# Kernel optimization log

Hardware: AMD Instinct MI355X
Metric: run time of the kernel (lower is better)

Reference implementation:

```python
import jax, jax.numpy as jnp
import numpy as np

D = 896      # mm_hidden_size
H = 8        # num heads
HD = D // H  # head dim = 112
M = 8        # num_memory_tokens
P = 196      # patch_size
EPS = 1e-12


def _layernorm(x, g, b):
    mu = jnp.mean(x, axis=-1, keepdims=True)
    var = jnp.mean(jnp.square(x - mu), axis=-1, keepdims=True)
    return (x - mu) * jax.lax.rsqrt(var + EPS) * g + b


def setup_inputs() -> dict:
    key = jax.random.key(0)
    ks = jax.random.split(key, 12)
    F = 32
    s = 0.02
    return {
        "image_features": jax.random.normal(ks[0], (F, P, D), jnp.float32),
        "initial_memory": jax.random.normal(ks[1], (M, P, D), jnp.float32),
        "qW": jax.random.normal(ks[2], (D, D), jnp.float32) * s,
        "qb": jnp.zeros((D,), jnp.float32),
        "kW": jax.random.normal(ks[3], (D, D), jnp.float32) * s,
        "kb": jnp.zeros((D,), jnp.float32),
        "vW": jax.random.normal(ks[4], (D, D), jnp.float32) * s,
        "vb": jnp.zeros((D,), jnp.float32),
        "oW": jax.random.normal(ks[5], (D, D), jnp.float32) * s,
        "ob": jnp.zeros((D,), jnp.float32),
        "ln1_g": jnp.ones((D,), jnp.float32),
        "ln1_b": jnp.zeros((D,), jnp.float32),
        "mW": jax.random.normal(ks[6], (D, 4 * D), jnp.float32) * s,
        "mb": jnp.zeros((4 * D,), jnp.float32),
        "pW": jax.random.normal(ks[7], (4 * D, D), jnp.float32) * s,
        "pb": jnp.zeros((D,), jnp.float32),
        "ln2_g": jnp.ones((D,), jnp.float32),
        "ln2_b": jnp.zeros((D,), jnp.float32),
    }


def reference(image_features, initial_memory, qW, qb, kW, kb, vW, vb,
              oW, ob, ln1_g, ln1_b, mW, mb, pW, pb, ln2_g, ln2_b):
    F = image_features.shape[0]
    Lq = M * P            # 1568 query tokens
    Lk = F * P            # kv tokens
    mem = initial_memory.reshape(1, Lq, D)      # [1, Lq, D]
    img = image_features.reshape(1, Lk, D)      # [1, Lk, D]

    def heads(x, L):
        return x.reshape(1, L, H, HD).transpose(0, 2, 1, 3)  # [1,H,L,hd]

    q = heads(mem @ qW + qb, Lq)
    k = heads(img @ kW + kb, Lk)
    v = heads(img @ vW + vb, Lk)

    scores = jnp.einsum('bhqd,bhkd->bhqk', q, k) / np.sqrt(HD).astype(jnp.float32)
    probs = jax.nn.softmax(scores, axis=-1)                  # [1,H,Lq,Lk]
    ctx = jnp.einsum('bhqk,bhkd->bhqd', probs, v)
    ctx = ctx.transpose(0, 2, 1, 3).reshape(1, Lq, D)

    # residual + layernorm epilogue of Attention
    attn_out = _layernorm(ctx @ oW + ob + mem, ln1_g, ln1_b)

    # MLP -> residual + layernorm
    hidden = jax.nn.relu(attn_out @ mW + mb)                 # [1, Lq, 4D]
    out = _layernorm(hidden @ pW + pb + attn_out, ln2_g, ln2_b)

    # frame attention scores: sum over heads and query tokens, avg per frame
    attn_sum = probs.sum(axis=(1, 2))[0]                     # [Lk]
    frame_scores = attn_sum.reshape(F, P).mean(axis=1)       # [F]

    final_memory = out.reshape(M, P, D)
    return final_memory, frame_scores
```

## Files before the change

kernel.cpp:

```cpp
#include <hip/hip_runtime.h>
#include <hip/hip_bf16.h>
#include <math.h>

#define TP_D   896
#define TP_H   8
#define TP_HD  112
#define TP_LQ  1568
#define TP_LK  6272
#define TP_D4  3584
#define TP_F   32
#define TP_P   196

typedef unsigned short u16;
typedef float f32x4 __attribute__((ext_vector_type(4)));
typedef __bf16 bf16x8 __attribute__((ext_vector_type(8)));

__device__ inline float bf2f(u16 u) {
    return __uint_as_float(((unsigned int)u) << 16);
}
__device__ inline u16 f2bf(float f) {
    unsigned int x = __float_as_uint(f);
    unsigned int lsb = (x >> 16) & 1u;
    x += 0x7fffu + lsb;
    return (u16)(x >> 16);
}
__device__ inline ushort4 pack4(float a, float b, float c, float d) {
    return make_ushort4(f2bf(a), f2bf(b), f2bf(c), f2bf(d));
}
__device__ inline int pidx(int row, int col) {
    return row * 128 + (col ^ ((row & 7) << 3));
}

__global__ void cast2_f32_bf16(const float* __restrict__ src0, u16* __restrict__ dst0, int n0,
                               const float* __restrict__ src1, u16* __restrict__ dst1, int n1) {
    int i = (blockIdx.x * blockDim.x + threadIdx.x) * 4;
    const float* s; u16* d; int n;
    if (i < n0) { s = src0; d = dst0; n = n0; }
    else        { i -= n0; s = src1; d = dst1; n = n1; if (i >= n) return; }
    float4 v = *(const float4*)(s + i);
    *(ushort4*)(d + i) = pack4(v.x, v.y, v.z, v.w);
}

__global__ void cast_div_bf16(const float* __restrict__ src, const float* __restrict__ l,
                              u16* __restrict__ dst) {
    int i = (blockIdx.x * 256 + threadIdx.x) * 4;
    if (i >= TP_LQ * TP_D) return;
    int q = i / TP_D;
    int col = i - q * TP_D;
    int h = col / TP_HD;
    float inv = 1.f / l[h * TP_LQ + q];
    float4 v = *(const float4*)(src + i);
    *(ushort4*)(dst + i) = pack4(v.x * inv, v.y * inv, v.z * inv, v.w * inv);
}

__global__ void transpose_cast(const float* __restrict__ src, u16* __restrict__ dst, int R, int C) {
    __shared__ float t[32][33];
    int bx = blockIdx.x * 32;
    int by = blockIdx.y * 32;
    int tx = threadIdx.x, ty = threadIdx.y;
#pragma unroll
    for (int j = 0; j < 4; ++j)
        t[ty + j * 8][tx] = src[(size_t)(by + ty + j * 8) * C + bx + tx];
    __syncthreads();
#pragma unroll
    for (int j = 0; j < 4; ++j)
        dst[(size_t)(bx + ty + j * 8) * R + by + tx] = f2bf(t[tx][ty + j * 8]);
}

struct GemmParams {
    const u16* A;  int lda;
    const u16* Bt; int ldb;
    int M, N, K;
    const float* bias;
    float* outF;
    u16* outB; int ldc;
    int relu;
    int kc;
};

#define LDS_STRIDE 56

template <int MODE, int NT>
__global__ __launch_bounds__(256, 4) void gemm_bf16(GemmParams p) {
    __shared__ u16 lsA[128 * LDS_STRIDE];
    __shared__ u16 lsB[NT * 32 * LDS_STRIDE];

    const int tid = threadIdx.x;
    const int z = blockIdx.z;
    const u16* A  = p.A;
    const u16* Bt = p.Bt;
    if (MODE == 6) {
        A  += (size_t)z * p.kc;
        Bt += (size_t)z * p.kc;
    }
    const int m0 = blockIdx.y * 128;
    const int n0 = blockIdx.x * (NT * 32);

    const int lane = tid & 63;
    const int w = tid >> 6;
    const int wm = (w >> 1) * 64, wn = (w & 1) * (16 * NT);
    const int c = lane & 15, q = lane >> 4;

    f32x4 acc[4][NT];
#pragma unroll
    for (int i = 0; i < 4; ++i)
#pragma unroll
        for (int j = 0; j < NT; ++j) acc[i][j] = 0.f;

    const int r0 = tid >> 2;
    const int c8 = (tid & 3) * 8;
    int arow0 = m0 + r0;      if (arow0 >= p.M) arow0 = p.M - 1;
    int arow1 = m0 + r0 + 64; if (arow1 >= p.M) arow1 = p.M - 1;
    int brow0 = n0 + r0;      if (brow0 >= p.N) brow0 = p.N - 1;
    int brow1 = n0 + r0 + 64; if (brow1 >= p.N) brow1 = p.N - 1;
    const u16* a0 = A  + (size_t)arow0 * p.lda + c8;
    const u16* a1 = A  + (size_t)arow1 * p.lda + c8;
    const u16* b0 = Bt + (size_t)brow0 * p.ldb + c8;
    const u16* b1 = Bt + (size_t)brow1 * p.ldb + c8;

    const int KT = (p.K + 31) >> 5;
    for (int kt = 0; kt < KT; ++kt) {
        const int k0 = kt << 5;
        const bool valid = (k0 + c8 + 8) <= p.K;
        uint4 zv = make_uint4(0, 0, 0, 0);
        uint4 va0 = valid ? *(const uint4*)(a0 + k0) : zv;
        uint4 va1 = valid ? *(const uint4*)(a1 + k0) : zv;
        uint4 vb0 = valid ? *(const uint4*)(b0 + k0) : zv;
        uint4 vb1 = (NT == 4 && valid) ? *(const uint4*)(b1 + k0) : zv;
        *(uint4*)(&lsA[r0 * LDS_STRIDE + c8])        = va0;
        *(uint4*)(&lsA[(r0 + 64) * LDS_STRIDE + c8]) = va1;
        *(uint4*)(&lsB[r0 * LDS_STRIDE + c8])        = vb0;
        if (NT == 4)
            *(uint4*)(&lsB[(r0 + 64) * LDS_STRIDE + c8]) = vb1;
        __syncthreads();

        bf16x8 af[4], bfv[NT];
#pragma unroll
        for (int mi = 0; mi < 4; ++mi)
            af[mi] = *(const bf16x8*)(&lsA[(wm + mi * 16 + c) * LDS_STRIDE + q * 8]);
#pragma unroll
        for (int ni = 0; ni < NT; ++ni)
            bfv[ni] = *(const bf16x8*)(&lsB[(wn + ni * 16 + c) * LDS_STRIDE + q * 8]);
#pragma unroll
        for (int mi = 0; mi < 4; ++mi)
#pragma unroll
            for (int ni = 0; ni < NT; ++ni)
                acc[mi][ni] = __builtin_amdgcn_mfma_f32_16x16x32_bf16(af[mi], bfv[ni], acc[mi][ni], 0, 0, 0);
        __syncthreads();
    }

    if (MODE == 7) {
#pragma unroll
        for (int ni = 0; ni < NT; ++ni) {
            const int col = n0 + wn + ni * 16 + c;
            const float bv = p.bias[col];
#pragma unroll
            for (int mi = 0; mi < 4; ++mi) {
                const int mbase = m0 + wm + mi * 16 + q * 4;
                f32x4 a = acc[mi][ni];
                *(ushort4*)(p.outB + (size_t)col * p.ldc + mbase) =
                    pack4(a[0] + bv, a[1] + bv, a[2] + bv, a[3] + bv);
            }
        }
        return;
    }

#pragma unroll
    for (int mi = 0; mi < 4; ++mi) {
#pragma unroll
        for (int r = 0; r < 4; ++r) {
            const int row = m0 + wm + mi * 16 + q * 4 + r;
            if (row >= p.M) continue;
#pragma unroll
            for (int ni = 0; ni < NT; ++ni) {
                const int col = n0 + wn + ni * 16 + c;
                float v = acc[mi][ni][r];
                if (MODE == 4) {
                    v += p.bias[col];
                    if (p.relu) v = v > 0.f ? v : 0.f;
                    p.outB[(size_t)row * p.ldc + col] = f2bf(v);
                } else if (MODE == 6) {
                    atomicAdd(&p.outF[(size_t)row * p.ldc + col], v);
                }
            }
        }
    }
}

__global__ __launch_bounds__(256, 2) void attn_fused(
        const u16* __restrict__ Qf, const u16* __restrict__ Kf,
        const u16* __restrict__ Vtf, u16* __restrict__ E,
        float* __restrict__ lsum, float* __restrict__ ctxF, float scale) {
    __shared__ u16 lsQ[128 * 128];
    __shared__ u16 lsB[128 * 40];
    __shared__ u16 lsP[128 * 128];

    const int ks  = blockIdx.x;
    const int m0  = blockIdx.y * 128;
    const int h   = blockIdx.z;
    const int tid = threadIdx.x;
    const int lane = tid & 63, w = tid >> 6;
    const int wm = (w >> 1) * 64, wn = (w & 1) * 64;
    const int c = lane & 15, q = lane >> 4;

    {
        const int row = tid >> 1;
        const int half = (tid & 1) * 64;
        int qrow = m0 + row; if (qrow > TP_LQ - 1) qrow = TP_LQ - 1;
        const u16* src = Qf + (size_t)qrow * TP_D + h * TP_HD;
#pragma unroll
        for (int j = 0; j < 8; ++j) {
            int col = half + j * 8;
            uint4 v = make_uint4(0, 0, 0, 0);
            if (col + 8 <= TP_HD) v = *(const uint4*)(src + col);
            *(uint4*)(&lsQ[pidx(row, col)]) = v;
        }
    }

    const int r0 = tid >> 2;
    const int c8 = (tid & 3) * 8;
    const int keybase = ks * 896;

    f32x4 acc_pv[4][4];
#pragma unroll
    for (int i = 0; i < 4; ++i)
#pragma unroll
        for (int j = 0; j < 4; ++j) acc_pv[i][j] = 0.f;
    float rs[4] = {0.f, 0.f, 0.f, 0.f};

    for (int kb = 0; kb < 7; ++kb) {
        const int kblk = keybase + kb * 128;
        f32x4 acc_s[4][4];
#pragma unroll
        for (int i = 0; i < 4; ++i)
#pragma unroll
            for (int j = 0; j < 4; ++j) acc_s[i][j] = 0.f;

#pragma unroll
        for (int kt = 0; kt < 4; ++kt) {
            const int k0 = kt * 32;
            const bool valid = (k0 + c8 + 8) <= TP_HD;
            uint4 zv = make_uint4(0, 0, 0, 0);
            uint4 vb0 = valid ? *(const uint4*)(Kf + (size_t)(kblk + r0) * TP_D + h * TP_HD + k0 + c8) : zv;
            uint4 vb1 = valid ? *(const uint4*)(Kf + (size_t)(kblk + r0 + 64) * TP_D + h * TP_HD + k0 + c8) : zv;
            __syncthreads();
            *(uint4*)(&lsB[r0 * 40 + c8])        = vb0;
            *(uint4*)(&lsB[(r0 + 64) * 40 + c8]) = vb1;
            __syncthreads();
            bf16x8 af[4], bfv[4];
#pragma unroll
            for (int mi = 0; mi < 4; ++mi)
                af[mi] = *(const bf16x8*)(&lsQ[pidx(wm + mi * 16 + c, k0 + q * 8)]);
#pragma unroll
            for (int ni = 0; ni < 4; ++ni)
                bfv[ni] = *(const bf16x8*)(&lsB[(wn + ni * 16 + c) * 40 + q * 8]);
#pragma unroll
            for (int mi = 0; mi < 4; ++mi)
#pragma unroll
                for (int ni = 0; ni < 4; ++ni)
                    acc_s[mi][ni] = __builtin_amdgcn_mfma_f32_16x16x32_bf16(bfv[ni], af[mi], acc_s[mi][ni], 0, 0, 0);
        }

        __syncthreads();
#pragma unroll
        for (int mi = 0; mi < 4; ++mi) {
            const int prow = wm + mi * 16 + c;
            const int qr = m0 + prow;
            const bool qv = qr < TP_LQ;
            float rp = 0.f;
#pragma unroll
            for (int ni = 0; ni < 4; ++ni) {
                float e0, e1, e2, e3;
                {
                    f32x4 a = acc_s[mi][ni];
                    e0 = __expf(fminf(a[0] * scale, 30.f));
                    e1 = __expf(fminf(a[1] * scale, 30.f));
                    e2 = __expf(fminf(a[2] * scale, 30.f));
                    e3 = __expf(fminf(a[3] * scale, 30.f));
                }
                rp += (e0 + e1) + (e2 + e3);
                ushort4 pk = pack4(e0, e1, e2, e3);
                const int kcol = wn + ni * 16 + q * 4;
                if (qv)
                    *(ushort4*)(E + ((size_t)h * TP_LQ + qr) * TP_LK + kblk + kcol) = pk;
                *(ushort4*)(&lsP[pidx(prow, kcol)]) = pk;
            }
            rs[mi] += rp;
        }

#pragma unroll
        for (int kt = 0; kt < 4; ++kt) {
            const int kk = kblk + kt * 32 + c8;
            int d0 = r0;
            int d1 = r0 + 64; if (d1 > TP_HD - 1) d1 = TP_HD - 1;
            uint4 vb0 = *(const uint4*)(Vtf + ((size_t)h * TP_HD + d0) * TP_LK + kk);
            uint4 vb1 = *(const uint4*)(Vtf + ((size_t)h * TP_HD + d1) * TP_LK + kk);
            __syncthreads();
            *(uint4*)(&lsB[r0 * 40 + c8])        = vb0;
            *(uint4*)(&lsB[(r0 + 64) * 40 + c8]) = vb1;
            __syncthreads();
            bf16x8 ap[4], bv[4];
#pragma unroll
            for (int mi = 0; mi < 4; ++mi)
                ap[mi] = *(const bf16x8*)(&lsP[pidx(wm + mi * 16 + c, kt * 32 + q * 8)]);
#pragma unroll
            for (int ni = 0; ni < 4; ++ni)
                bv[ni] = *(const bf16x8*)(&lsB[(wn + ni * 16 + c) * 40 + q * 8]);
#pragma unroll
            for (int mi = 0; mi < 4; ++mi)
#pragma unroll
                for (int ni = 0; ni < 4; ++ni)
                    acc_pv[mi][ni] = __builtin_amdgcn_mfma_f32_16x16x32_bf16(ap[mi], bv[ni], acc_pv[mi][ni], 0, 0, 0);
        }
    }

#pragma unroll
    for (int mi = 0; mi < 4; ++mi) {
        float rp = rs[mi];
        rp += __shfl_xor(rp, 16, 64);
        rp += __shfl_xor(rp, 32, 64);
        const int qr = m0 + wm + mi * 16 + c;
        if (q == 0 && qr < TP_LQ) atomicAdd(&lsum[h * TP_LQ + qr], rp);
    }
#pragma unroll
    for (int mi = 0; mi < 4; ++mi) {
#pragma unroll
        for (int r = 0; r < 4; ++r) {
            const int qr = m0 + wm + mi * 16 + q * 4 + r;
            if (qr >= TP_LQ) continue;
#pragma unroll
            for (int ni = 0; ni < 4; ++ni) {
                const int d = wn + ni * 16 + c;
                if (d < TP_HD)
                    atomicAdd(&ctxF[(size_t)qr * TP_D + h * TP_HD + d], acc_pv[mi][ni][r]);
            }
        }
    }
}

__global__ void colsum_kernel(const u16* __restrict__ E, const float* __restrict__ l,
                              float* __restrict__ colsum, int nrows) {
    int c4 = blockIdx.x * 256 + threadIdx.x;
    if (c4 >= TP_LK / 4) return;
    int chunk = (nrows + gridDim.y - 1) / gridDim.y;
    int r0 = blockIdx.y * chunk;
    int r1 = r0 + chunk; if (r1 > nrows) r1 = nrows;
    float a0 = 0.f, a1 = 0.f, a2 = 0.f, a3 = 0.f;
    for (int r = r0; r < r1; ++r) {
        float inv = 1.f / l[r];
        ushort4 u = ((const ushort4*)(E + (size_t)r * TP_LK))[c4];
        a0 += bf2f(u.x) * inv; a1 += bf2f(u.y) * inv;
        a2 += bf2f(u.z) * inv; a3 += bf2f(u.w) * inv;
    }
    atomicAdd(&colsum[4 * c4 + 0], a0);
    atomicAdd(&colsum[4 * c4 + 1], a1);
    atomicAdd(&colsum[4 * c4 + 2], a2);
    atomicAdd(&colsum[4 * c4 + 3], a3);
}

__global__ __launch_bounds__(256) void layernorm_rows(const float* __restrict__ x,
        const float* __restrict__ bias, const float* __restrict__ res,
        const float* __restrict__ g, const float* __restrict__ b,
        float* __restrict__ outF, u16* __restrict__ outB) {
    const int tid = threadIdx.x;
    const float* xr = x + (size_t)blockIdx.x * TP_D;
    const float* rr = res + (size_t)blockIdx.x * TP_D;
    float v[4];
#pragma unroll
    for (int i = 0; i < 4; ++i) {
        int idx = tid + i * 256;
        v[i] = (idx < TP_D) ? (xr[idx] + bias[idx] + rr[idx]) : 0.f;
    }
    float s = v[0] + v[1] + v[2] + v[3];
    __shared__ float red[4];
#pragma unroll
    for (int o = 32; o > 0; o >>= 1) s += __shfl_xor(s, o, 64);
    if ((tid & 63) == 0) red[tid >> 6] = s;
    __syncthreads();
    const float mu = (red[0] + red[1] + red[2] + red[3]) * (1.f / TP_D);
    __syncthreads();
    float ss = 0.f;
#pragma unroll
    for (int i = 0; i < 4; ++i) {
        int idx = tid + i * 256;
        if (idx < TP_D) { float d = v[i] - mu; ss += d * d; }
    }
#pragma unroll
    for (int o = 32; o > 0; o >>= 1) ss += __shfl_xor(ss, o, 64);
    if ((tid & 63) == 0) red[tid >> 6] = ss;
    __syncthreads();
    const float var = (red[0] + red[1] + red[2] + red[3]) * (1.f / TP_D);
    const float rsq = rsqrtf(var + 1e-12f);
    float* of = outF + (size_t)blockIdx.x * TP_D;
    u16* obp = outB ? outB + (size_t)blockIdx.x * TP_D : nullptr;
#pragma unroll
    for (int i = 0; i < 4; ++i) {
        int idx = tid + i * 256;
        if (idx < TP_D) {
            float y = (v[i] - mu) * rsq * g[idx] + b[idx];
            of[idx] = y;
            if (obp) obp[idx] = f2bf(y);
        }
    }
}

__global__ void frame_scores_kernel(const float* __restrict__ colsum, float* __restrict__ out) {
    const int tid = threadIdx.x;
    float v = (tid < TP_P) ? colsum[blockIdx.x * TP_P + tid] : 0.f;
    __shared__ float red[4];
#pragma unroll
    for (int o = 32; o > 0; o >>= 1) v += __shfl_xor(v, o, 64);
    if ((tid & 63) == 0) red[tid >> 6] = v;
    __syncthreads();
    if (tid == 0) out[blockIdx.x] = (red[0] + red[1] + red[2] + red[3]) * (1.f / TP_P);
}

extern "C" void kernel_launch(void* const* d_in, const int* in_sizes, int n_in,
                              void* d_out, int out_size, void* d_ws, size_t ws_size,
                              hipStream_t stream) {
    const float* img  = (const float*)d_in[0];
    const float* mem  = (const float*)d_in[1];
    const float* qW   = (const float*)d_in[2];
    const float* qb   = (const float*)d_in[3];
    const float* kW   = (const float*)d_in[4];
    const float* kb   = (const float*)d_in[5];
    const float* vW   = (const float*)d_in[6];
    const float* vb   = (const float*)d_in[7];
    const float* oW   = (const float*)d_in[8];
    const float* ob   = (const float*)d_in[9];
    const float* ln1g = (const float*)d_in[10];
    const float* ln1b = (const float*)d_in[11];
    const float* mW   = (const float*)d_in[12];
    const float* mb   = (const float*)d_in[13];
    const float* pW   = (const float*)d_in[14];
    const float* pb   = (const float*)d_in[15];
    const float* ln2g = (const float*)d_in[16];
    const float* ln2b = (const float*)d_in[17];
    float* out = (float*)d_out;

    char* base = (char*)d_ws;
    size_t off = 0;
    auto take = [&](size_t nbytes) -> void* {
        void* p = base + off;
        off += (nbytes + 255) & ~(size_t)255;
        return p;
    };

    u16* imgB  = (u16*)take((size_t)TP_LK * TP_D * 2);
    u16* memB  = (u16*)take((size_t)TP_LQ * TP_D * 2);
    u16* qWt   = (u16*)take((size_t)TP_D * TP_D * 2);
    u16* kWt   = (u16*)take((size_t)TP_D * TP_D * 2);
    u16* vWt   = (u16*)take((size_t)TP_D * TP_D * 2);
    u16* oWt   = (u16*)take((size_t)TP_D * TP_D * 2);
    u16* mWt   = (u16*)take((size_t)TP_D * TP_D4 * 2);
    u16* pWt   = (u16*)take((size_t)TP_D * TP_D4 * 2);
    u16* Qf    = (u16*)take((size_t)TP_LQ * TP_D * 2);
    u16* Kf    = (u16*)take((size_t)TP_LK * TP_D * 2);
    u16* Vtf   = (u16*)take((size_t)TP_LK * TP_D * 2);
    u16* ctxB  = (u16*)take((size_t)TP_LQ * TP_D * 2);
    float* attn  = (float*)take((size_t)TP_LQ * TP_D * 4);
    u16* attnB = (u16*)take((size_t)TP_LQ * TP_D * 2);
    u16* hidden= (u16*)take((size_t)TP_LQ * TP_D4 * 2);
    u16* E     = (u16*)take((size_t)TP_H * TP_LQ * TP_LK * 2);
    float* ctxF  = (float*)take((size_t)TP_LQ * TP_D * 4);
    float* pre1  = (float*)take((size_t)TP_LQ * TP_D * 4);
    float* pre2  = (float*)take((size_t)TP_LQ * TP_D * 4);
    float* colsum= (float*)take((size_t)TP_LK * 4);
    float* lsum  = (float*)take((size_t)TP_H * TP_LQ * 4);
    size_t zlen = (char*)(lsum + TP_H * TP_LQ) - (char*)ctxF;

    {
        int n0 = TP_LK * TP_D, n1 = TP_LQ * TP_D;
        cast2_f32_bf16<<<((n0 + n1) / 4 + 255) / 256, 256, 0, stream>>>(img, imgB, n0, mem, memB, n1);
    }
    transpose_cast<<<dim3(28, 28), dim3(32, 8), 0, stream>>>(qW, qWt, TP_D, TP_D);
    transpose_cast<<<dim3(28, 28), dim3(32, 8), 0, stream>>>(kW, kWt, TP_D, TP_D);
    transpose_cast<<<dim3(28, 28), dim3(32, 8), 0, stream>>>(vW, vWt, TP_D, TP_D);
    transpose_cast<<<dim3(28, 28), dim3(32, 8), 0, stream>>>(oW, oWt, TP_D, TP_D);
    transpose_cast<<<dim3(TP_D4 / 32, TP_D / 32), dim3(32, 8), 0, stream>>>(mW, mWt, TP_D, TP_D4);
    transpose_cast<<<dim3(TP_D / 32, TP_D4 / 32), dim3(32, 8), 0, stream>>>(pW, pWt, TP_D4, TP_D);
    hipMemsetAsync(ctxF, 0, zlen, stream);

    {
        GemmParams p{};
        p.A = memB; p.lda = TP_D;
        p.Bt = qWt; p.ldb = TP_D;
        p.M = TP_LQ; p.N = TP_D; p.K = TP_D;
        p.bias = qb; p.outB = Qf; p.ldc = TP_D; p.relu = 0;
        gemm_bf16<4, 2><<<dim3(14, 13, 1), 256, 0, stream>>>(p);
    }
    {
        GemmParams p{};
        p.A = imgB; p.lda = TP_D;
        p.Bt = kWt; p.ldb = TP_D;
        p.M = TP_LK; p.N = TP_D; p.K = TP_D;
        p.bias = kb; p.outB = Kf; p.ldc = TP_D; p.relu = 0;
        gemm_bf16<4, 2><<<dim3(14, 49, 1), 256, 0, stream>>>(p);
    }
    {
        GemmParams p{};
        p.A = imgB; p.lda = TP_D;
        p.Bt = vWt; p.ldb = TP_D;
        p.M = TP_LK; p.N = TP_D; p.K = TP_D;
        p.bias = vb; p.outB = Vtf; p.ldc = TP_LK;
        gemm_bf16<7, 2><<<dim3(14, 49, 1), 256, 0, stream>>>(p);
    }

    const float scale = 0.09449111825230679f;
    attn_fused<<<dim3(7, 13, TP_H), 256, 0, stream>>>(Qf, Kf, Vtf, E, lsum, ctxF, scale);
    colsum_kernel<<<dim3(7, 224), 256, 0, stream>>>(E, lsum, colsum, TP_H * TP_LQ);
    cast_div_bf16<<<(TP_LQ * TP_D / 4 + 255) / 256, 256, 0, stream>>>(ctxF, lsum, ctxB);

    {
        GemmParams p{};
        p.A = ctxB; p.lda = TP_D;
        p.Bt = oWt; p.ldb = TP_D;
        p.M = TP_LQ; p.N = TP_D; p.K = 448; p.kc = 448;
        p.outF = pre1; p.ldc = TP_D;
        gemm_bf16<6, 2><<<dim3(14, 13, 2), 256, 0, stream>>>(p);
    }
    layernorm_rows<<<TP_LQ, 256, 0, stream>>>(pre1, ob, mem, ln1g, ln1b, attn, attnB);

    {
        GemmParams p{};
        p.A = attnB; p.lda = TP_D;
        p.Bt = mWt; p.ldb = TP_D;
        p.M = TP_LQ; p.N = TP_D4; p.K = TP_D;
        p.bias = mb; p.outB = hidden; p.ldc = TP_D4; p.relu = 1;
        gemm_bf16<4, 2><<<dim3(56, 13, 1), 256, 0, stream>>>(p);
    }
    {
        GemmParams p{};
        p.A = hidden; p.lda = TP_D4;
        p.Bt = pWt; p.ldb = TP_D4;
        p.M = TP_LQ; p.N = TP_D; p.K = 896; p.kc = 896;
        p.outF = pre2; p.ldc = TP_D;
        gemm_bf16<6, 2><<<dim3(14, 13, 4), 256, 0, stream>>>(p);
    }
    layernorm_rows<<<TP_LQ, 256, 0, stream>>>(pre2, pb, attn, ln2g, ln2b, out, nullptr);

    frame_scores_kernel<<<TP_F, 256, 0, stream>>>(colsum, out + (size_t)TP_LQ * TP_D);
}
```

Before: 543.6 us.

## Keep Q fragments in registers and stage full K/V tiles once per key block

The attention kernel now loads the per-warp Q fragments straight into registers once, instead of staging Q in shared memory. It also loads each full 128-key K tile and V tile into one shared buffer per key block rather than in four 32-wide slices. This cuts the __syncthreads barriers per key block from about 16 to 4 and removes the repeated Q reads from LDS. In exchange it uses more registers (16 bf16x8 Q fragments per thread), which may hurt occupancy at 2 blocks per CU. The colsum launch grid is also doubled along y.

```diff
diff --git a/kernel.cpp b/kernel.cpp
--- a/kernel.cpp
+++ b/kernel.cpp
@@ -191,8 +191,7 @@
         const u16* __restrict__ Qf, const u16* __restrict__ Kf,
         const u16* __restrict__ Vtf, u16* __restrict__ E,
         float* __restrict__ lsum, float* __restrict__ ctxF, float scale) {
-    __shared__ u16 lsQ[128 * 128];
-    __shared__ u16 lsB[128 * 40];
+    __shared__ u16 lsKV[128 * 128];
     __shared__ u16 lsP[128 * 128];
 
     const int ks  = blockIdx.x;
@@ -203,22 +202,21 @@
     const int wm = (w >> 1) * 64, wn = (w & 1) * 64;
     const int c = lane & 15, q = lane >> 4;
 
-    {
-        const int row = tid >> 1;
-        const int half = (tid & 1) * 64;
-        int qrow = m0 + row; if (qrow > TP_LQ - 1) qrow = TP_LQ - 1;
-        const u16* src = Qf + (size_t)qrow * TP_D + h * TP_HD;
-#pragma unroll
-        for (int j = 0; j < 8; ++j) {
-            int col = half + j * 8;
-            uint4 v = make_uint4(0, 0, 0, 0);
-            if (col + 8 <= TP_HD) v = *(const uint4*)(src + col);
-            *(uint4*)(&lsQ[pidx(row, col)]) = v;
-        }
-    }
-
-    const int r0 = tid >> 2;
-    const int c8 = (tid & 3) * 8;
+    bf16x8 qf[4][4];
+#pragma unroll
+    for (int mi = 0; mi < 4; ++mi) {
+        int qr = m0 + wm + mi * 16 + c; if (qr > TP_LQ - 1) qr = TP_LQ - 1;
+        const u16* src = Qf + (size_t)qr * TP_D + h * TP_HD;
+#pragma unroll
+        for (int kt = 0; kt < 4; ++kt) {
+            int d0 = kt * 32 + q * 8;
+            if (d0 + 8 <= TP_HD) qf[mi][kt] = *(const bf16x8*)(src + d0);
+            else { union { int4 i; bf16x8 v; } u; u.i = make_int4(0, 0, 0, 0); qf[mi][kt] = u.v; }
+        }
+    }
+
+    const int srow = tid >> 1;
+    const int shalf = (tid & 1) * 64;
     const int keybase = ks * 896;
 
     f32x4 acc_pv[4][4];
@@ -230,38 +228,37 @@
 
     for (int kb = 0; kb < 7; ++kb) {
         const int kblk = keybase + kb * 128;
+
+        {
+            const u16* src = Kf + (size_t)(kblk + srow) * TP_D + h * TP_HD;
+#pragma unroll
+            for (int j = 0; j < 8; ++j) {
+                int col = shalf + j * 8;
+                uint4 v = make_uint4(0, 0, 0, 0);
+                if (col + 8 <= TP_HD) v = *(const uint4*)(src + col);
+                *(uint4*)(&lsKV[pidx(srow, col)]) = v;
+            }
+        }
+        __syncthreads();
+
         f32x4 acc_s[4][4];
 #pragma unroll
         for (int i = 0; i < 4; ++i)
 #pragma unroll
             for (int j = 0; j < 4; ++j) acc_s[i][j] = 0.f;
-
 #pragma unroll
         for (int kt = 0; kt < 4; ++kt) {
-            const int k0 = kt * 32;
-            const bool valid = (k0 + c8 + 8) <= TP_HD;
-            uint4 zv = make_uint4(0, 0, 0, 0);
-            uint4 vb0 = valid ? *(const uint4*)(Kf + (size_t)(kblk + r0) * TP_D + h * TP_HD + k0 + c8) : zv;
-            uint4 vb1 = valid ? *(const uint4*)(Kf + (size_t)(kblk + r0 + 64) * TP_D + h * TP_HD + k0 + c8) : zv;
-            __syncthreads();
-            *(uint4*)(&lsB[r0 * 40 + c8])        = vb0;
-            *(uint4*)(&lsB[(r0 + 64) * 40 + c8]) = vb1;
-            __syncthreads();
-            bf16x8 af[4], bfv[4];
+            bf16x8 kf[4];
+#pragma unroll
+            for (int ni = 0; ni < 4; ++ni)
+                kf[ni] = *(const bf16x8*)(&lsKV[pidx(wn + ni * 16 + c, kt * 32 + q * 8)]);
 #pragma unroll
             for (int mi = 0; mi < 4; ++mi)
-                af[mi] = *(const bf16x8*)(&lsQ[pidx(wm + mi * 16 + c, k0 + q * 8)]);
-#pragma unroll
-            for (int ni = 0; ni < 4; ++ni)
-                bfv[ni] = *(const bf16x8*)(&lsB[(wn + ni * 16 + c) * 40 + q * 8]);
-#pragma unroll
-            for (int mi = 0; mi < 4; ++mi)
 #pragma unroll
                 for (int ni = 0; ni < 4; ++ni)
-                    acc_s[mi][ni] = __builtin_amdgcn_mfma_f32_16x16x32_bf16(bfv[ni], af[mi], acc_s[mi][ni], 0, 0, 0);
-        }
-
-        __syncthreads();
+                    acc_s[mi][ni] = __builtin_amdgcn_mfma_f32_16x16x32_bf16(kf[ni], qf[mi][kt], acc_s[mi][ni], 0, 0, 0);
+        }
+
 #pragma unroll
         for (int mi = 0; mi < 4; ++mi) {
             const int prow = wm + mi * 16 + c;
@@ -270,14 +267,11 @@
             float rp = 0.f;
 #pragma unroll
             for (int ni = 0; ni < 4; ++ni) {
-                float e0, e1, e2, e3;
-                {
-                    f32x4 a = acc_s[mi][ni];
-                    e0 = __expf(fminf(a[0] * scale, 30.f));
-                    e1 = __expf(fminf(a[1] * scale, 30.f));
-                    e2 = __expf(fminf(a[2] * scale, 30.f));
-                    e3 = __expf(fminf(a[3] * scale, 30.f));
-                }
+                f32x4 a = acc_s[mi][ni];
+                float e0 = __expf(fminf(a[0] * scale, 30.f));
+                float e1 = __expf(fminf(a[1] * scale, 30.f));
+                float e2 = __expf(fminf(a[2] * scale, 30.f));
+                float e3 = __expf(fminf(a[3] * scale, 30.f));
                 rp += (e0 + e1) + (e2 + e3);
                 ushort4 pk = pack4(e0, e1, e2, e3);
                 const int kcol = wn + ni * 16 + q * 4;
@@ -287,31 +281,36 @@
             }
             rs[mi] += rp;
         }
+        __syncthreads();
+
+        {
+            uint4 zv = make_uint4(0, 0, 0, 0);
+            const u16* src = Vtf + ((size_t)h * TP_HD + srow) * TP_LK + kblk;
+#pragma unroll
+            for (int j = 0; j < 8; ++j) {
+                int col = shalf + j * 8;
+                uint4 v = (srow < TP_HD) ? *(const uint4*)(src + col) : zv;
+                *(uint4*)(&lsKV[pidx(srow, col)]) = v;
+            }
+        }
+        __syncthreads();
 
 #pragma unroll
         for (int kt = 0; kt < 4; ++kt) {
-            const int kk = kblk + kt * 32 + c8;
-            int d0 = r0;
-            int d1 = r0 + 64; if (d1 > TP_HD - 1) d1 = TP_HD - 1;
-            uint4 vb0 = *(const uint4*)(Vtf + ((size_t)h * TP_HD + d0) * TP_LK + kk);
-            uint4 vb1 = *(const uint4*)(Vtf + ((size_t)h * TP_HD + d1) * TP_LK + kk);
-            __syncthreads();
-            *(uint4*)(&lsB[r0 * 40 + c8])        = vb0;
-            *(uint4*)(&lsB[(r0 + 64) * 40 + c8]) = vb1;
-            __syncthreads();
             bf16x8 ap[4], bv[4];
 #pragma unroll
             for (int mi = 0; mi < 4; ++mi)
                 ap[mi] = *(const bf16x8*)(&lsP[pidx(wm + mi * 16 + c, kt * 32 + q * 8)]);
 #pragma unroll
             for (int ni = 0; ni < 4; ++ni)
-                bv[ni] = *(const bf16x8*)(&lsB[(wn + ni * 16 + c) * 40 + q * 8]);
+                bv[ni] = *(const bf16x8*)(&lsKV[pidx(wn + ni * 16 + c, kt * 32 + q * 8)]);
 #pragma unroll
             for (int mi = 0; mi < 4; ++mi)
 #pragma unroll
                 for (int ni = 0; ni < 4; ++ni)
                     acc_pv[mi][ni] = __builtin_amdgcn_mfma_f32_16x16x32_bf16(ap[mi], bv[ni], acc_pv[mi][ni], 0, 0, 0);
         }
+        __syncthreads();
     }
 
 #pragma unroll
@@ -508,7 +507,7 @@
 
     const float scale = 0.09449111825230679f;
     attn_fused<<<dim3(7, 13, TP_H), 256, 0, stream>>>(Qf, Kf, Vtf, E, lsum, ctxF, scale);
-    colsum_kernel<<<dim3(7, 224), 256, 0, stream>>>(E, lsum, colsum, TP_H * TP_LQ);
+    colsum_kernel<<<dim3(7, 448), 256, 0, stream>>>(E, lsum, colsum, TP_H * TP_LQ);
     cast_div_bf16<<<(TP_LQ * TP_D / 4 + 255) / 256, 256, 0, stream>>>(ctxF, lsum, ctxB);
 
     {
```

Measured after the change: 661.6 us. 1.22x slower.
